# Kernel optimization log

Measured on AMD Instinct MI355X. Metric: run time of the kernel, lower is better.

Reference implementation:

```python
import jax, jax.numpy as jnp
import numpy as np

N_HEADS, D_MODEL, D_HEAD = 16, 1024, 64
BATCH, SEQ = 2, 2048
INIT_RANGE = 0.02


def setup_inputs() -> dict:
    key = jax.random.key(0)
    ks = jax.random.split(key, 5)
    x = jax.random.normal(ks[0], (BATCH, SEQ, D_MODEL), dtype=jnp.float32)
    W_Q = jax.random.normal(ks[1], (N_HEADS, D_MODEL, D_HEAD), dtype=jnp.float32) * INIT_RANGE
    W_K = jax.random.normal(ks[2], (N_HEADS, D_MODEL, D_HEAD), dtype=jnp.float32) * INIT_RANGE
    W_V = jax.random.normal(ks[3], (N_HEADS, D_MODEL, D_HEAD), dtype=jnp.float32) * INIT_RANGE
    W_O = jax.random.normal(ks[4], (N_HEADS, D_HEAD, D_MODEL), dtype=jnp.float32) * INIT_RANGE
    b_Q = jnp.zeros((N_HEADS, D_HEAD), dtype=jnp.float32)
    b_K = jnp.zeros((N_HEADS, D_HEAD), dtype=jnp.float32)
    b_V = jnp.zeros((N_HEADS, D_HEAD), dtype=jnp.float32)
    b_O = jnp.zeros((D_MODEL,), dtype=jnp.float32)
    return {"normalized_resid_pre": x, "W_Q": W_Q, "W_K": W_K, "W_V": W_V,
            "W_O": W_O, "b_Q": b_Q, "b_K": b_K, "b_V": b_V, "b_O": b_O}


def reference(normalized_resid_pre, W_Q, W_K, W_V, W_O, b_Q, b_K, b_V, b_O):
    x = normalized_resid_pre  # [b, s, d_model]
    q = jnp.einsum('bsm,hmd->bshd', x, W_Q) + b_Q  # [b, s, h, d_head]
    k = jnp.einsum('bsm,hmd->bshd', x, W_K) + b_K
    v = jnp.einsum('bsm,hmd->bshd', x, W_V) + b_V
    scores = jnp.einsum('bqhd,bkhd->bhqk', q, k) / jnp.sqrt(jnp.float32(D_HEAD))
    seq = x.shape[1]
    causal = jnp.tril(jnp.ones((seq, seq), dtype=bool))  # True where allowed
    scores = jnp.where(causal, scores, jnp.float32(-jnp.inf))
    pattern = jax.nn.softmax(scores, axis=-1)  # [b, h, q, k]
    z = jnp.einsum('bhqk,bkhd->bqhd', pattern, v)
    attn_out = jnp.einsum('bqhd,hdm->bqm', z, W_O) + b_O
    return attn_out
```

## Files before the change

### kernel.cpp

```cpp
#include <hip/hip_runtime.h>
#include <hip/hip_bf16.h>

#define BATCH 2
#define SEQL 2048
#define NH 16
#define DH 64
#define DM 1024
#define LDK 72
#define QSCALE 0.1803368801111244f

typedef __hip_bfloat16 bf16;
typedef __attribute__((ext_vector_type(8))) short  bf16x8;
typedef __attribute__((ext_vector_type(4))) float  f32x4;

__device__ __forceinline__ void gl_lds16(const void* g, void* l) {
    __builtin_amdgcn_global_load_lds(
        (const __attribute__((address_space(1))) unsigned int*)g,
        (__attribute__((address_space(3))) unsigned int*)l, 16, 0, 0);
}

__global__ __launch_bounds__(256) void xconv_kernel(
    const float* __restrict__ x, bf16* __restrict__ xb)
{
    const size_t i = ((size_t)blockIdx.x * 256 + threadIdx.x) * 4;
    const float4 v = *(const float4*)(x + i);
    bf16 o[4];
    o[0] = __float2bfloat16(v.x); o[1] = __float2bfloat16(v.y);
    o[2] = __float2bfloat16(v.z); o[3] = __float2bfloat16(v.w);
    *(uint2*)(xb + i) = *(const uint2*)o;
}

__global__ __launch_bounds__(256) void wtrans_kernel(
    const float* __restrict__ Wq, const float* __restrict__ Wk,
    const float* __restrict__ Wv, const float* __restrict__ Wo,
    bf16* __restrict__ Wt)
{
    __shared__ float ts[64][65];
    const int zi = blockIdx.z;
    const float* src = (zi == 0) ? Wq : (zi == 1) ? Wk : (zi == 2) ? Wv : Wo;
    bf16* dst = Wt + (size_t)zi * DM * DM;
    const int row0 = blockIdx.y * 64;
    const int col0 = blockIdx.x * 64;
    const int tx = threadIdx.x & 63;
    const int ty = threadIdx.x >> 6;

    if (zi < 3) {
        const int h = col0 >> 6;
        #pragma unroll
        for (int i = 0; i < 16; ++i) {
            const int r = ty + 4 * i;
            ts[r][tx] = src[h * (DM * DH) + (row0 + r) * DH + tx];
        }
    } else {
        #pragma unroll
        for (int i = 0; i < 16; ++i) {
            const int r = ty + 4 * i;
            ts[r][tx] = src[(size_t)(row0 + r) * DM + col0 + tx];
        }
    }
    __syncthreads();
    #pragma unroll
    for (int i = 0; i < 16; ++i) {
        const int rr = ty + 4 * i;
        dst[(size_t)(col0 + rr) * DM + row0 + tx] = __float2bfloat16(ts[tx][rr]);
    }
}

__global__ __launch_bounds__(256) void qkv_gemm(
    const bf16* __restrict__ xb, const bf16* __restrict__ Wt,
    const float* __restrict__ bq, const float* __restrict__ bk, const float* __restrict__ bv,
    bf16* __restrict__ qkv)
{
    __shared__ __align__(16) bf16 As[128 * 32];
    __shared__ __align__(16) bf16 Bs[128 * 32];

    const int t = threadIdx.x;
    const int lane = t & 63, w = t >> 6;
    const int ml = lane & 15, quad = lane >> 4;
    const int wr = w >> 1, wc = w & 1;
    const int bn = blockIdx.x, bm = blockIdx.y, which = blockIdx.z;

    const bf16* A0 = xb + (size_t)(bm * 128) * DM;
    const bf16* B0 = Wt + (size_t)which * DM * DM + (size_t)(bn * 128) * DM;
    const float* bias = (which == 0) ? bq : (which == 1) ? bk : bv;
    bf16* outb = qkv + (size_t)which * (BATCH * SEQL * NH * DH);
    const float oscale = (which == 0) ? QSCALE : 1.0f;

    f32x4 acc[4][4];
    #pragma unroll
    for (int i = 0; i < 4; ++i)
        #pragma unroll
        for (int j = 0; j < 4; ++j) acc[i][j] = (f32x4){0.f, 0.f, 0.f, 0.f};

    for (int kt = 0; kt < DM / 32; ++kt) {
        const int k0 = kt * 32;
        __syncthreads();
        #pragma unroll
        for (int j = 0; j < 2; ++j) {
            const int flat = t + j * 256;
            const int r = flat >> 2, c = (flat & 3) * 8;
            gl_lds16(A0 + (size_t)r * DM + k0 + c, &As[flat * 8]);
            gl_lds16(B0 + (size_t)r * DM + k0 + c, &Bs[flat * 8]);
        }
        __syncthreads();
        bf16x8 af[4], bfr[4];
        #pragma unroll
        for (int i = 0; i < 4; ++i)
            af[i] = *(const bf16x8*)&As[(wr * 64 + i * 16 + ml) * 32 + quad * 8];
        #pragma unroll
        for (int j = 0; j < 4; ++j)
            bfr[j] = *(const bf16x8*)&Bs[(wc * 64 + j * 16 + ml) * 32 + quad * 8];
        #pragma unroll
        for (int i = 0; i < 4; ++i)
            #pragma unroll
            for (int j = 0; j < 4; ++j)
                acc[i][j] = __builtin_amdgcn_mfma_f32_16x16x32_bf16(af[i], bfr[j], acc[i][j], 0, 0, 0);
    }

    float bb[4];
    #pragma unroll
    for (int j = 0; j < 4; ++j) bb[j] = bias[bn * 128 + wc * 64 + j * 16 + ml];

    #pragma unroll
    for (int i = 0; i < 4; ++i) {
        #pragma unroll
        for (int rg = 0; rg < 4; ++rg) {
            const int row = bm * 128 + wr * 64 + i * 16 + quad * 4 + rg;
            const int b = row >> 11;
            const int s = row & (SEQL - 1);
            #pragma unroll
            for (int j = 0; j < 4; ++j) {
                const int col = bn * 128 + wc * 64 + j * 16 + ml;
                const int h = col >> 6, d = col & 63;
                const bf16 val = __float2bfloat16((acc[i][j][rg] + bb[j]) * oscale);
                if (which == 2)
                    outb[(((size_t)(b * NH + h)) * DH + d) * SEQL + s] = val;
                else
                    outb[(((size_t)(b * NH + h)) * SEQL + s) * DH + d] = val;
            }
        }
    }
}

__global__ __launch_bounds__(256) void oproj_gemm(
    const bf16* __restrict__ zb, const bf16* __restrict__ Bt,
    const float* __restrict__ bo, float* __restrict__ out)
{
    __shared__ __align__(16) bf16 As[128 * 32];
    __shared__ __align__(16) bf16 Bs[128 * 32];

    const int t = threadIdx.x;
    const int lane = t & 63, w = t >> 6;
    const int ml = lane & 15, quad = lane >> 4;
    const int wr = w >> 1, wc = w & 1;
    const int bn = blockIdx.x, bm = blockIdx.y;

    const bf16* A0 = zb + (size_t)(bm * 128) * DM;
    const bf16* B0 = Bt + (size_t)(bn * 128) * DM;

    f32x4 acc[4][4];
    #pragma unroll
    for (int i = 0; i < 4; ++i)
        #pragma unroll
        for (int j = 0; j < 4; ++j) acc[i][j] = (f32x4){0.f, 0.f, 0.f, 0.f};

    for (int kt = 0; kt < DM / 32; ++kt) {
        const int k0 = kt * 32;
        __syncthreads();
        #pragma unroll
        for (int j = 0; j < 2; ++j) {
            const int flat = t + j * 256;
            const int r = flat >> 2, c = (flat & 3) * 8;
            gl_lds16(A0 + (size_t)r * DM + k0 + c, &As[flat * 8]);
            gl_lds16(B0 + (size_t)r * DM + k0 + c, &Bs[flat * 8]);
        }
        __syncthreads();
        bf16x8 af[4], bfr[4];
        #pragma unroll
        for (int i = 0; i < 4; ++i)
            af[i] = *(const bf16x8*)&As[(wr * 64 + i * 16 + ml) * 32 + quad * 8];
        #pragma unroll
        for (int j = 0; j < 4; ++j)
            bfr[j] = *(const bf16x8*)&Bs[(wc * 64 + j * 16 + ml) * 32 + quad * 8];
        #pragma unroll
        for (int i = 0; i < 4; ++i)
            #pragma unroll
            for (int j = 0; j < 4; ++j)
                acc[i][j] = __builtin_amdgcn_mfma_f32_16x16x32_bf16(af[i], bfr[j], acc[i][j], 0, 0, 0);
    }

    float bb[4];
    #pragma unroll
    for (int j = 0; j < 4; ++j) bb[j] = bo[bn * 128 + wc * 64 + j * 16 + ml];

    #pragma unroll
    for (int i = 0; i < 4; ++i) {
        #pragma unroll
        for (int rg = 0; rg < 4; ++rg) {
            const int row = bm * 128 + wr * 64 + i * 16 + quad * 4 + rg;
            #pragma unroll
            for (int j = 0; j < 4; ++j) {
                const int col = bn * 128 + wc * 64 + j * 16 + ml;
                out[(size_t)row * DM + col] = acc[i][j][rg] + bb[j];
            }
        }
    }
}

__global__ __launch_bounds__(256) void attn_kernel(
    const bf16* __restrict__ qg, const bf16* __restrict__ kg, const bf16* __restrict__ vtg,
    bf16* __restrict__ z)
{
    __shared__ bf16 KsS[64 * LDK];
    __shared__ bf16 VtS[64 * LDK];
    __shared__ bf16 PsS[4][16 * LDK];

    const int t    = threadIdx.x;
    const int lane = t & 63;
    const int w    = t >> 6;
    const int m    = lane & 15;
    const int quad = lane >> 4;

    const int bh = blockIdx.x;
    const int b  = bh >> 4;
    const int h  = bh & 15;
    const int qt = (gridDim.y - 1) - blockIdx.y;
    const int q0 = qt * 64;

    const size_t base = (size_t)bh * SEQL * DH;
    const size_t vtbase = (size_t)bh * DH * SEQL;

    const int rp = t >> 3;
    const int d0 = (t & 7) * 8;

    bf16x8 aq[2];
    {
        const bf16* qp = qg + base + (size_t)(q0 + w * 16 + m) * DH + quad * 8;
        aq[0] = *(const bf16x8*)(qp);
        aq[1] = *(const bf16x8*)(qp + 32);
    }

    const short ob = (m == 0) ? (short)0x3F80 : (short)0;
    const bf16x8 bones = {ob, ob, ob, ob, ob, ob, ob, ob};

    f32x4 zacc[4];
    #pragma unroll
    for (int nt = 0; nt < 4; ++nt) zacc[nt] = (f32x4){0.f, 0.f, 0.f, 0.f};
    f32x4 lacc = (f32x4){0.f, 0.f, 0.f, 0.f};

    bf16* Psw = PsS[w];

    for (int kt = 0; kt <= qt; ++kt) {
        __syncthreads();
        {
            const bf16* kr = kg + base + (size_t)(kt * 64 + 2 * rp) * DH + d0;
            const bf16* vr = vtg + vtbase + (size_t)(2 * rp) * SEQL + kt * 64 + d0;
            const uint4 k0 = *(const uint4*)(kr);
            const uint4 k1 = *(const uint4*)(kr + DH);
            const uint4 v0 = *(const uint4*)(vr);
            const uint4 v1 = *(const uint4*)(vr + SEQL);
            *(uint4*)(&KsS[(2 * rp) * LDK + d0])     = k0;
            *(uint4*)(&KsS[(2 * rp + 1) * LDK + d0]) = k1;
            *(uint4*)(&VtS[(2 * rp) * LDK + d0])     = v0;
            *(uint4*)(&VtS[(2 * rp + 1) * LDK + d0]) = v1;
        }
        __syncthreads();

        f32x4 sc[4];
        #pragma unroll
        for (int nt = 0; nt < 4; ++nt) sc[nt] = (f32x4){0.f, 0.f, 0.f, 0.f};
        #pragma unroll
        for (int ks = 0; ks < 2; ++ks) {
            #pragma unroll
            for (int nt = 0; nt < 4; ++nt) {
                const bf16x8 bk = *(const bf16x8*)(&KsS[(nt * 16 + m) * LDK + ks * 32 + quad * 8]);
                sc[nt] = __builtin_amdgcn_mfma_f32_16x16x32_bf16(aq[ks], bk, sc[nt], 0, 0, 0);
            }
        }
        if (kt == qt) {
            #pragma unroll
            for (int nt = 0; nt < 4; ++nt) {
                const int col = nt * 16 + m;
                #pragma unroll
                for (int rg = 0; rg < 4; ++rg) {
                    const int row = w * 16 + quad * 4 + rg;
                    if (col > row) sc[nt][rg] = -1e30f;
                }
            }
        }

        #pragma unroll
        for (int nt = 0; nt < 4; ++nt)
            #pragma unroll
            for (int rg = 0; rg < 4; ++rg)
                Psw[(quad * 4 + rg) * LDK + nt * 16 + m] =
                    __float2bfloat16(__builtin_exp2f(sc[nt][rg]));

        #pragma unroll
        for (int ks = 0; ks < 2; ++ks) {
            const bf16x8 ap = *(const bf16x8*)(&Psw[m * LDK + ks * 32 + quad * 8]);
            lacc = __builtin_amdgcn_mfma_f32_16x16x32_bf16(ap, bones, lacc, 0, 0, 0);
            #pragma unroll
            for (int nt = 0; nt < 4; ++nt) {
                const bf16x8 bv = *(const bf16x8*)(&VtS[(nt * 16 + m) * LDK + ks * 32 + quad * 8]);
                zacc[nt] = __builtin_amdgcn_mfma_f32_16x16x32_bf16(ap, bv, zacc[nt], 0, 0, 0);
            }
        }
    }

    float invl[4];
    #pragma unroll
    for (int rg = 0; rg < 4; ++rg)
        invl[rg] = 1.f / __shfl(lacc[rg], quad * 16);
    #pragma unroll
    for (int nt = 0; nt < 4; ++nt) {
        const int d = nt * 16 + m;
        #pragma unroll
        for (int rg = 0; rg < 4; ++rg) {
            const int qrow = q0 + w * 16 + quad * 4 + rg;
            z[(((size_t)b * SEQL + qrow) * NH + h) * DH + d] =
                __float2bfloat16(zacc[nt][rg] * invl[rg]);
        }
    }
}

extern "C" void kernel_launch(void* const* d_in, const int* in_sizes, int n_in,
                              void* d_out, int out_size, void* d_ws, size_t ws_size,
                              hipStream_t stream)
{
    const float* x  = (const float*)d_in[0];
    const float* Wq = (const float*)d_in[1];
    const float* Wk = (const float*)d_in[2];
    const float* Wv = (const float*)d_in[3];
    const float* Wo = (const float*)d_in[4];
    const float* bq = (const float*)d_in[5];
    const float* bk = (const float*)d_in[6];
    const float* bv = (const float*)d_in[7];
    const float* bo = (const float*)d_in[8];
    float* out = (float*)d_out;

    const size_t TOK = (size_t)BATCH * SEQL;
    const size_t QKV = TOK * DM;
    bf16* xb  = (bf16*)d_ws;
    bf16* Wt  = xb + QKV;
    bf16* qkv = Wt + 4 * (size_t)DM * DM;
    bf16* zb  = qkv + 3 * QKV;

    xconv_kernel<<<dim3(TOK * DM / 1024), 256, 0, stream>>>(x, xb);
    wtrans_kernel<<<dim3(16, 16, 4), 256, 0, stream>>>(Wq, Wk, Wv, Wo, Wt);
    qkv_gemm<<<dim3(8, 32, 3), 256, 0, stream>>>(xb, Wt, bq, bk, bv, qkv);
    attn_kernel<<<dim3(BATCH * NH, SEQL / 64), 256, 0, stream>>>(
        qkv, qkv + QKV, qkv + 2 * QKV, zb);
    oproj_gemm<<<dim3(8, 32), 256, 0, stream>>>(zb, Wt + 3 * (size_t)DM * DM, bo, out);
}
```

Before: 200.9 us.

## Use persistent atomic-counter scheduling for attention and narrow oproj tiles

The attention kernel becomes persistent: 512 blocks pull (query-tile, head) tasks from a global atomic counter, longest causal tiles first, so load balances across the triangular workload. The O-projection GEMM tile is narrowed from 128 to 64 columns, doubling its grid for better CU occupancy. The V-transpose epilogue in the QKV GEMM now writes four consecutive bf16 values as one 8-byte store instead of scalar stores. The added memset and atomics add small overhead, and the V path drops the oscale factor, which is fine only if oscale is 1 for V.

```diff
diff --git a/kernel.cpp b/kernel.cpp
--- a/kernel.cpp
+++ b/kernel.cpp
@@ -8,6 +8,7 @@
 #define DM 1024
 #define LDK 72
 #define QSCALE 0.1803368801111244f
+#define NTASKS 1024u
 
 typedef __hip_bfloat16 bf16;
 typedef __attribute__((ext_vector_type(8))) short  bf16x8;
@@ -121,22 +122,39 @@
     #pragma unroll
     for (int j = 0; j < 4; ++j) bb[j] = bias[bn * 128 + wc * 64 + j * 16 + ml];
 
-    #pragma unroll
-    for (int i = 0; i < 4; ++i) {
-        #pragma unroll
-        for (int rg = 0; rg < 4; ++rg) {
-            const int row = bm * 128 + wr * 64 + i * 16 + quad * 4 + rg;
-            const int b = row >> 11;
-            const int s = row & (SEQL - 1);
+    if (which == 2) {
+        #pragma unroll
+        for (int i = 0; i < 4; ++i) {
+            const int row0v = bm * 128 + wr * 64 + i * 16 + quad * 4;
+            const int b = row0v >> 11;
+            const int s0 = row0v & (SEQL - 1);
             #pragma unroll
             for (int j = 0; j < 4; ++j) {
                 const int col = bn * 128 + wc * 64 + j * 16 + ml;
                 const int h = col >> 6, d = col & 63;
-                const bf16 val = __float2bfloat16((acc[i][j][rg] + bb[j]) * oscale);
-                if (which == 2)
-                    outb[(((size_t)(b * NH + h)) * DH + d) * SEQL + s] = val;
-                else
-                    outb[(((size_t)(b * NH + h)) * SEQL + s) * DH + d] = val;
+                bf16 tmp[4];
+                #pragma unroll
+                for (int rg = 0; rg < 4; ++rg)
+                    tmp[rg] = __float2bfloat16(acc[i][j][rg] + bb[j]);
+                *(uint2*)&outb[(((size_t)(b * NH + h)) * DH + d) * SEQL + s0] =
+                    *(const uint2*)tmp;
+            }
+        }
+    } else {
+        #pragma unroll
+        for (int i = 0; i < 4; ++i) {
+            #pragma unroll
+            for (int rg = 0; rg < 4; ++rg) {
+                const int row = bm * 128 + wr * 64 + i * 16 + quad * 4 + rg;
+                const int b = row >> 11;
+                const int s = row & (SEQL - 1);
+                #pragma unroll
+                for (int j = 0; j < 4; ++j) {
+                    const int col = bn * 128 + wc * 64 + j * 16 + ml;
+                    const int h = col >> 6, d = col & 63;
+                    outb[(((size_t)(b * NH + h)) * SEQL + s) * DH + d] =
+                        __float2bfloat16((acc[i][j][rg] + bb[j]) * oscale);
+                }
             }
         }
     }
@@ -147,7 +165,7 @@
     const float* __restrict__ bo, float* __restrict__ out)
 {
     __shared__ __align__(16) bf16 As[128 * 32];
-    __shared__ __align__(16) bf16 Bs[128 * 32];
+    __shared__ __align__(16) bf16 Bs[64 * 32];
 
     const int t = threadIdx.x;
     const int lane = t & 63, w = t >> 6;
@@ -156,42 +174,43 @@
     const int bn = blockIdx.x, bm = blockIdx.y;
 
     const bf16* A0 = zb + (size_t)(bm * 128) * DM;
-    const bf16* B0 = Bt + (size_t)(bn * 128) * DM;
-
-    f32x4 acc[4][4];
+    const bf16* B0 = Bt + (size_t)(bn * 64) * DM;
+
+    f32x4 acc[4][2];
     #pragma unroll
     for (int i = 0; i < 4; ++i)
         #pragma unroll
-        for (int j = 0; j < 4; ++j) acc[i][j] = (f32x4){0.f, 0.f, 0.f, 0.f};
+        for (int j = 0; j < 2; ++j) acc[i][j] = (f32x4){0.f, 0.f, 0.f, 0.f};
 
     for (int kt = 0; kt < DM / 32; ++kt) {
         const int k0 = kt * 32;
         __syncthreads();
-        #pragma unroll
-        for (int j = 0; j < 2; ++j) {
-            const int flat = t + j * 256;
-            const int r = flat >> 2, c = (flat & 3) * 8;
-            gl_lds16(A0 + (size_t)r * DM + k0 + c, &As[flat * 8]);
-            gl_lds16(B0 + (size_t)r * DM + k0 + c, &Bs[flat * 8]);
-        }
-        __syncthreads();
-        bf16x8 af[4], bfr[4];
+        {
+            const int r0 = t >> 2, c0 = (t & 3) * 8;
+            gl_lds16(A0 + (size_t)r0 * DM + k0 + c0, &As[t * 8]);
+            const int f1 = t + 256;
+            const int r1 = f1 >> 2, c1 = (f1 & 3) * 8;
+            gl_lds16(A0 + (size_t)r1 * DM + k0 + c1, &As[f1 * 8]);
+            gl_lds16(B0 + (size_t)r0 * DM + k0 + c0, &Bs[t * 8]);
+        }
+        __syncthreads();
+        bf16x8 af[4], bfr[2];
         #pragma unroll
         for (int i = 0; i < 4; ++i)
             af[i] = *(const bf16x8*)&As[(wr * 64 + i * 16 + ml) * 32 + quad * 8];
         #pragma unroll
-        for (int j = 0; j < 4; ++j)
-            bfr[j] = *(const bf16x8*)&Bs[(wc * 64 + j * 16 + ml) * 32 + quad * 8];
+        for (int j = 0; j < 2; ++j)
+            bfr[j] = *(const bf16x8*)&Bs[(wc * 32 + j * 16 + ml) * 32 + quad * 8];
         #pragma unroll
         for (int i = 0; i < 4; ++i)
             #pragma unroll
-            for (int j = 0; j < 4; ++j)
+            for (int j = 0; j < 2; ++j)
                 acc[i][j] = __builtin_amdgcn_mfma_f32_16x16x32_bf16(af[i], bfr[j], acc[i][j], 0, 0, 0);
     }
 
-    float bb[4];
-    #pragma unroll
-    for (int j = 0; j < 4; ++j) bb[j] = bo[bn * 128 + wc * 64 + j * 16 + ml];
+    float bb[2];
+    #pragma unroll
+    for (int j = 0; j < 2; ++j) bb[j] = bo[bn * 64 + wc * 32 + j * 16 + ml];
 
     #pragma unroll
     for (int i = 0; i < 4; ++i) {
@@ -199,8 +218,8 @@
         for (int rg = 0; rg < 4; ++rg) {
             const int row = bm * 128 + wr * 64 + i * 16 + quad * 4 + rg;
             #pragma unroll
-            for (int j = 0; j < 4; ++j) {
-                const int col = bn * 128 + wc * 64 + j * 16 + ml;
+            for (int j = 0; j < 2; ++j) {
+                const int col = bn * 64 + wc * 32 + j * 16 + ml;
                 out[(size_t)row * DM + col] = acc[i][j][rg] + bb[j];
             }
         }
@@ -209,11 +228,12 @@
 
 __global__ __launch_bounds__(256) void attn_kernel(
     const bf16* __restrict__ qg, const bf16* __restrict__ kg, const bf16* __restrict__ vtg,
-    bf16* __restrict__ z)
+    bf16* __restrict__ z, unsigned* __restrict__ counter)
 {
     __shared__ bf16 KsS[64 * LDK];
     __shared__ bf16 VtS[64 * LDK];
     __shared__ bf16 PsS[4][16 * LDK];
+    __shared__ unsigned taskS;
 
     const int t    = threadIdx.x;
     const int lane = t & 63;
@@ -221,105 +241,113 @@
     const int m    = lane & 15;
     const int quad = lane >> 4;
 
-    const int bh = blockIdx.x;
-    const int b  = bh >> 4;
-    const int h  = bh & 15;
-    const int qt = (gridDim.y - 1) - blockIdx.y;
-    const int q0 = qt * 64;
-
-    const size_t base = (size_t)bh * SEQL * DH;
-    const size_t vtbase = (size_t)bh * DH * SEQL;
-
     const int rp = t >> 3;
     const int d0 = (t & 7) * 8;
 
-    bf16x8 aq[2];
-    {
-        const bf16* qp = qg + base + (size_t)(q0 + w * 16 + m) * DH + quad * 8;
-        aq[0] = *(const bf16x8*)(qp);
-        aq[1] = *(const bf16x8*)(qp + 32);
-    }
-
     const short ob = (m == 0) ? (short)0x3F80 : (short)0;
     const bf16x8 bones = {ob, ob, ob, ob, ob, ob, ob, ob};
 
-    f32x4 zacc[4];
-    #pragma unroll
-    for (int nt = 0; nt < 4; ++nt) zacc[nt] = (f32x4){0.f, 0.f, 0.f, 0.f};
-    f32x4 lacc = (f32x4){0.f, 0.f, 0.f, 0.f};
-
     bf16* Psw = PsS[w];
 
-    for (int kt = 0; kt <= qt; ++kt) {
-        __syncthreads();
+    for (;;) {
+        __syncthreads();
+        if (t == 0) taskS = atomicAdd(counter, 1u);
+        __syncthreads();
+        const unsigned task = taskS;
+        if (task >= NTASKS) break;
+
+        const int qt = 31 - (int)(task >> 5);
+        const int bh = (int)(task & 31u);
+        const int b  = bh >> 4;
+        const int h  = bh & 15;
+        const int q0 = qt * 64;
+
+        const size_t base   = (size_t)bh * SEQL * DH;
+        const size_t vtbase = (size_t)bh * DH * SEQL;
+
+        bf16x8 aq[2];
         {
-            const bf16* kr = kg + base + (size_t)(kt * 64 + 2 * rp) * DH + d0;
-            const bf16* vr = vtg + vtbase + (size_t)(2 * rp) * SEQL + kt * 64 + d0;
-            const uint4 k0 = *(const uint4*)(kr);
-            const uint4 k1 = *(const uint4*)(kr + DH);
-            const uint4 v0 = *(const uint4*)(vr);
-            const uint4 v1 = *(const uint4*)(vr + SEQL);
-            *(uint4*)(&KsS[(2 * rp) * LDK + d0])     = k0;
-            *(uint4*)(&KsS[(2 * rp + 1) * LDK + d0]) = k1;
-            *(uint4*)(&VtS[(2 * rp) * LDK + d0])     = v0;
-            *(uint4*)(&VtS[(2 * rp + 1) * LDK + d0]) = v1;
-        }
-        __syncthreads();
-
-        f32x4 sc[4];
-        #pragma unroll
-        for (int nt = 0; nt < 4; ++nt) sc[nt] = (f32x4){0.f, 0.f, 0.f, 0.f};
-        #pragma unroll
-        for (int ks = 0; ks < 2; ++ks) {
-            #pragma unroll
-            for (int nt = 0; nt < 4; ++nt) {
-                const bf16x8 bk = *(const bf16x8*)(&KsS[(nt * 16 + m) * LDK + ks * 32 + quad * 8]);
-                sc[nt] = __builtin_amdgcn_mfma_f32_16x16x32_bf16(aq[ks], bk, sc[nt], 0, 0, 0);
-            }
-        }
-        if (kt == qt) {
-            #pragma unroll
-            for (int nt = 0; nt < 4; ++nt) {
-                const int col = nt * 16 + m;
-                #pragma unroll
-                for (int rg = 0; rg < 4; ++rg) {
-                    const int row = w * 16 + quad * 4 + rg;
-                    if (col > row) sc[nt][rg] = -1e30f;
+            const bf16* qp = qg + base + (size_t)(q0 + w * 16 + m) * DH + quad * 8;
+            aq[0] = *(const bf16x8*)(qp);
+            aq[1] = *(const bf16x8*)(qp + 32);
+        }
+
+        f32x4 zacc[4];
+        #pragma unroll
+        for (int nt = 0; nt < 4; ++nt) zacc[nt] = (f32x4){0.f, 0.f, 0.f, 0.f};
+        f32x4 lacc = (f32x4){0.f, 0.f, 0.f, 0.f};
+
+        for (int kt = 0; kt <= qt; ++kt) {
+            __syncthreads();
+            {
+                const bf16* kr = kg + base + (size_t)(kt * 64 + 2 * rp) * DH + d0;
+                const bf16* vr = vtg + vtbase + (size_t)(2 * rp) * SEQL + kt * 64 + d0;
+                const uint4 k0 = *(const uint4*)(kr);
+                const uint4 k1 = *(const uint4*)(kr + DH);
+                const uint4 v0 = *(const uint4*)(vr);
+                const uint4 v1 = *(const uint4*)(vr + SEQL);
+                *(uint4*)(&KsS[(2 * rp) * LDK + d0])     = k0;
+                *(uint4*)(&KsS[(2 * rp + 1) * LDK + d0]) = k1;
+                *(uint4*)(&VtS[(2 * rp) * LDK + d0])     = v0;
+                *(uint4*)(&VtS[(2 * rp + 1) * LDK + d0]) = v1;
+            }
+            __syncthreads();
+
+            f32x4 sc[4];
+            #pragma unroll
+            for (int nt = 0; nt < 4; ++nt) sc[nt] = (f32x4){0.f, 0.f, 0.f, 0.f};
+            #pragma unroll
+            for (int ks = 0; ks < 2; ++ks) {
+                #pragma unroll
+                for (int nt = 0; nt < 4; ++nt) {
+                    const bf16x8 bk = *(const bf16x8*)(&KsS[(nt * 16 + m) * LDK + ks * 32 + quad * 8]);
+                    sc[nt] = __builtin_amdgcn_mfma_f32_16x16x32_bf16(aq[ks], bk, sc[nt], 0, 0, 0);
                 }
             }
-        }
-
-        #pragma unroll
-        for (int nt = 0; nt < 4; ++nt)
-            #pragma unroll
-            for (int rg = 0; rg < 4; ++rg)
-                Psw[(quad * 4 + rg) * LDK + nt * 16 + m] =
-                    __float2bfloat16(__builtin_exp2f(sc[nt][rg]));
-
-        #pragma unroll
-        for (int ks = 0; ks < 2; ++ks) {
-            const bf16x8 ap = *(const bf16x8*)(&Psw[m * LDK + ks * 32 + quad * 8]);
-            lacc = __builtin_amdgcn_mfma_f32_16x16x32_bf16(ap, bones, lacc, 0, 0, 0);
-            #pragma unroll
-            for (int nt = 0; nt < 4; ++nt) {
-                const bf16x8 bv = *(const bf16x8*)(&VtS[(nt * 16 + m) * LDK + ks * 32 + quad * 8]);
-                zacc[nt] = __builtin_amdgcn_mfma_f32_16x16x32_bf16(ap, bv, zacc[nt], 0, 0, 0);
-            }
-        }
-    }
-
-    float invl[4];
-    #pragma unroll
-    for (int rg = 0; rg < 4; ++rg)
-        invl[rg] = 1.f / __shfl(lacc[rg], quad * 16);
-    #pragma unroll
-    for (int nt = 0; nt < 4; ++nt) {
-        const int d = nt * 16 + m;
-        #pragma unroll
-        for (int rg = 0; rg < 4; ++rg) {
-            const int qrow = q0 + w * 16 + quad * 4 + rg;
-            z[(((size_t)b * SEQL + qrow) * NH + h) * DH + d] =
-                __float2bfloat16(zacc[nt][rg] * invl[rg]);
+            if (kt == qt) {
+                #pragma unroll
+                for (int nt = 0; nt < 4; ++nt) {
+                    const int col = nt * 16 + m;
+                    #pragma unroll
+                    for (int rg = 0; rg < 4; ++rg) {
+                        const int row = w * 16 + quad * 4 + rg;
+                        if (col > row) sc[nt][rg] = -1e30f;
+                    }
+                }
+            }
+
+            #pragma unroll
+            for (int nt = 0; nt < 4; ++nt)
+                #pragma unroll
+                for (int rg = 0; rg < 4; ++rg)
+                    Psw[(quad * 4 + rg) * LDK + nt * 16 + m] =
+                        __float2bfloat16(__builtin_exp2f(sc[nt][rg]));
+
+            #pragma unroll
+            for (int ks = 0; ks < 2; ++ks) {
+                const bf16x8 ap = *(const bf16x8*)(&Psw[m * LDK + ks * 32 + quad * 8]);
+                lacc = __builtin_amdgcn_mfma_f32_16x16x32_bf16(ap, bones, lacc, 0, 0, 0);
+                #pragma unroll
+                for (int nt = 0; nt < 4; ++nt) {
+                    const bf16x8 bv = *(const bf16x8*)(&VtS[(nt * 16 + m) * LDK + ks * 32 + quad * 8]);
+                    zacc[nt] = __builtin_amdgcn_mfma_f32_16x16x32_bf16(ap, bv, zacc[nt], 0, 0, 0);
+                }
+            }
+        }
+
+        float invl[4];
+        #pragma unroll
+        for (int rg = 0; rg < 4; ++rg)
+            invl[rg] = 1.f / __shfl(lacc[rg], quad * 16);
+        #pragma unroll
+        for (int nt = 0; nt < 4; ++nt) {
+            const int d = nt * 16 + m;
+            #pragma unroll
+            for (int rg = 0; rg < 4; ++rg) {
+                const int qrow = q0 + w * 16 + quad * 4 + rg;
+                z[(((size_t)b * SEQL + qrow) * NH + h) * DH + d] =
+                    __float2bfloat16(zacc[nt][rg] * invl[rg]);
+            }
         }
     }
 }
@@ -345,11 +373,13 @@
     bf16* Wt  = xb + QKV;
     bf16* qkv = Wt + 4 * (size_t)DM * DM;
     bf16* zb  = qkv + 3 * QKV;
-
+    unsigned* counter = (unsigned*)(zb + QKV);
+
+    hipMemsetAsync(counter, 0, sizeof(unsigned), stream);
     xconv_kernel<<<dim3(TOK * DM / 1024), 256, 0, stream>>>(x, xb);
     wtrans_kernel<<<dim3(16, 16, 4), 256, 0, stream>>>(Wq, Wk, Wv, Wo, Wt);
     qkv_gemm<<<dim3(8, 32, 3), 256, 0, stream>>>(xb, Wt, bq, bk, bv, qkv);
-    attn_kernel<<<dim3(BATCH * NH, SEQL / 64), 256, 0, stream>>>(
-        qkv, qkv + QKV, qkv + 2 * QKV, zb);
-    oproj_gemm<<<dim3(8, 32), 256, 0, stream>>>(zb, Wt + 3 * (size_t)DM * DM, bo, out);
-}
+    attn_kernel<<<dim3(512), 256, 0, stream>>>(
+        qkv, qkv + QKV, qkv + 2 * QKV, zb, counter);
+    oproj_gemm<<<dim3(16, 32), 256, 0, stream>>>(zb, Wt + 3 * (size_t)DM * DM, bo, out);
+}
```

Result: slower. 205.5 us (+2.3%).
